# Performance work log

Hardware: AMD Instinct MI355X
Metric: run time of the kernel (lower is better)

The kernel has to match this reference:

```python
import jax, jax.numpy as jnp
import numpy as np

NUM_USERS = 100_000
NUM_ITEMS = 50_000
D = 64           # input_dim
K = 3            # num_weights (basis diagonal weights)
C = 5            # num_classes
E = 2_000_000    # number of (user, item) edges


def setup_inputs() -> dict:
    key = jax.random.key(0)
    ks = jax.random.split(key, 8)
    he = np.sqrt(2.0 / D).astype(np.float32)  # he_normal scale for [*, D] weights
    return {
        "u_feat": jax.random.normal(ks[0], (NUM_USERS, D), dtype=jnp.float32),
        "v_feat": jax.random.normal(ks[1], (NUM_ITEMS, D), dtype=jnp.float32),
        "W": jax.random.normal(ks[2], (K, D), dtype=jnp.float32) * he,
        "scalars": jax.random.normal(ks[3], (K, C), dtype=jnp.float32) * np.sqrt(2.0 / K).astype(np.float32),
        "u_bias": jnp.zeros((NUM_USERS, C), dtype=jnp.float32) + 0.01 * jax.random.normal(ks[4], (NUM_USERS, C), dtype=jnp.float32),
        "v_bias": jnp.zeros((NUM_ITEMS, C), dtype=jnp.float32) + 0.01 * jax.random.normal(ks[5], (NUM_ITEMS, C), dtype=jnp.float32),
        "u_idx": jax.random.randint(ks[6], (E,), 0, NUM_USERS, dtype=jnp.int32),
        "v_idx": jax.random.randint(ks[7], (E,), 0, NUM_ITEMS, dtype=jnp.int32),
    }


def reference(u_feat, v_feat, W, scalars, u_bias, v_bias, u_idx, v_idx):
    # Gather per-edge user/item embedding rows: [E, D]
    u_g = u_feat[u_idx]
    v_g = v_feat[v_idx]
    # Diagonal bilinear form per basis k: sum_d u_d * W[k,d] * v_d
    # = (u * v) @ W^T  -> basis_outputs: [E, K]
    basis_outputs = (u_g * v_g) @ W.T
    # Combine bases into class logits: [E, C]
    outputs = basis_outputs @ scalars
    # user_item_bias=True: add gathered per-user / per-item class biases
    outputs = outputs + u_bias[u_idx] + v_bias[v_idx]
    # activation=None -> linear
    return outputs
```

## Files before the change

### kernel.cpp

```cpp
#include <hip/hip_runtime.h>


template <int CTRL>
__device__ __forceinline__ float dpp_add(float x) {
    int t = __builtin_amdgcn_update_dpp(0, __float_as_int(x), CTRL, 0xF, 0xF, true);
    return x + __int_as_float(t);
}
template <int CTRL>
__device__ __forceinline__ float dpp_max(float x) {
    int t = __builtin_amdgcn_update_dpp(0, __float_as_int(x), CTRL, 0xF, 0xF, true);
    return fmaxf(x, __int_as_float(t));
}

__device__ __forceinline__ void reduce16_3(float& a, float& b, float& c) {
    a = dpp_add<0xB1>(a);  b = dpp_add<0xB1>(b);  c = dpp_add<0xB1>(c);
    a = dpp_add<0x4E>(a);  b = dpp_add<0x4E>(b);  c = dpp_add<0x4E>(c);
    a = dpp_add<0x124>(a); b = dpp_add<0x124>(b); c = dpp_add<0x124>(c);
    a = dpp_add<0x128>(a); b = dpp_add<0x128>(b); c = dpp_add<0x128>(c);
}
__device__ __forceinline__ float reduce16_max(float x) {
    x = dpp_max<0xB1>(x); x = dpp_max<0x4E>(x);
    x = dpp_max<0x124>(x); x = dpp_max<0x128>(x);
    return x;
}

__global__ __launch_bounds__(256) void quantize_tables_i8(
    const float* __restrict__ u_feat, const float* __restrict__ v_feat,
    int* __restrict__ u_q, int* __restrict__ v_q,
    float* __restrict__ u_s, float* __restrict__ v_s,
    int nrow_u, int nrow_v)
{
    const int tid   = blockIdx.x * blockDim.x + threadIdx.x;
    const int sl    = threadIdx.x & 15;
    const int group = tid >> 4;
    const int ng    = (gridDim.x * blockDim.x) >> 4;
    const int ntot  = nrow_u + nrow_v;

    for (int r = group; r < ntot; r += ng) {
        const bool  isU = (r < nrow_u);
        const int   rr  = isU ? r : r - nrow_u;
        const float* src = (isU ? u_feat : v_feat) + (size_t)rr * 64 + sl * 4;
        const float4 x = *reinterpret_cast<const float4*>(src);

        float am = fmaxf(fmaxf(fabsf(x.x), fabsf(x.y)),
                         fmaxf(fabsf(x.z), fabsf(x.w)));
        am = reduce16_max(am);
        am = fmaxf(am, 1e-20f);
        const float inv   = 127.0f / am;
        const float scale = am / 127.0f;

        const int b0 = (int)rintf(x.x * inv);
        const int b1 = (int)rintf(x.y * inv);
        const int b2 = (int)rintf(x.z * inv);
        const int b3 = (int)rintf(x.w * inv);
        const int packed = (b0 & 255) | ((b1 & 255) << 8) |
                           ((b2 & 255) << 16) | ((b3 & 255) << 24);

        (isU ? u_q : v_q)[(size_t)rr * 16 + sl] = packed;
        if (sl == 0) (isU ? u_s : v_s)[rr] = scale;
    }
}

__device__ __forceinline__ void unpack4(int t, float& f0, float& f1, float& f2, float& f3) {
    f0 = (float)((t << 24) >> 24);
    f1 = (float)((t << 16) >> 24);
    f2 = (float)((t <<  8) >> 24);
    f3 = (float)( t        >> 24);
}

__global__ __launch_bounds__(256) void bilinear_edges_i8(
    const int* __restrict__ u_q, const int* __restrict__ v_q,
    const float* __restrict__ u_s, const float* __restrict__ v_s,
    const float* __restrict__ W, const float* __restrict__ scalars,
    const float* __restrict__ u_bias, const float* __restrict__ v_bias,
    const int* __restrict__ u_idx, const int* __restrict__ v_idx,
    float* __restrict__ out, int E)
{
    const int tid    = blockIdx.x * blockDim.x + threadIdx.x;
    const int sl     = threadIdx.x & 15;
    const int group  = tid >> 4;
    const int ngroup = (gridDim.x * blockDim.x) >> 4;
    const int step   = ngroup * 2;

    const int d0 = sl * 4;
    float w0[4], w1[4], w2[4];
    #pragma unroll
    for (int j = 0; j < 4; ++j) {
        w0[j] = W[0 * 64 + d0 + j];
        w1[j] = W[1 * 64 + d0 + j];
        w2[j] = W[2 * 64 + d0 + j];
    }
    float s0 = 0.f, s1 = 0.f, s2 = 0.f;
    if (sl < 5) { s0 = scalars[0 * 5 + sl]; s1 = scalars[1 * 5 + sl]; s2 = scalars[2 * 5 + sl]; }

    int e0 = group * 2;
    if (e0 >= E) return;

    int uu0 = u_idx[e0];
    int vv0 = v_idx[e0];
    int uu1 = (e0 + 1 < E) ? u_idx[e0 + 1] : uu0;
    int vv1 = (e0 + 1 < E) ? v_idx[e0 + 1] : vv0;

    for (; e0 < E; e0 += step) {
        const int  e1   = e0 + 1;
        const bool has1 = (e1 < E);
        const int cu0 = uu0, cv0 = vv0, cu1 = uu1, cv1 = vv1;

        const int qu0 = u_q[(size_t)cu0 * 16 + sl];
        const int qv0 = v_q[(size_t)cv0 * 16 + sl];
        const int qu1 = u_q[(size_t)cu1 * 16 + sl];
        const int qv1 = v_q[(size_t)cv1 * 16 + sl];

        const int en = e0 + step;
        if (en < E) {
            uu0 = u_idx[en];
            vv0 = v_idx[en];
            const int en1 = en + 1;
            uu1 = (en1 < E) ? u_idx[en1] : uu0;
            vv1 = (en1 < E) ? v_idx[en1] : vv0;
        }

        float ub0 = 0.f, vb0 = 0.f, ub1 = 0.f, vb1 = 0.f;
        float ss0 = 0.f, ss1 = 0.f;
        if (sl < 5) {
            ss0 = u_s[cu0] * v_s[cv0];
            ss1 = u_s[cu1] * v_s[cv1];
            ub0 = u_bias[(size_t)cu0 * 5 + sl];
            vb0 = v_bias[(size_t)cv0 * 5 + sl];
            ub1 = u_bias[(size_t)cu1 * 5 + sl];
            vb1 = v_bias[(size_t)cv1 * 5 + sl];
        }

        float ua0, ua1, ua2, ua3, va0, va1, va2, va3;
        float ub0f, ub1f, ub2f, ub3f, vb0f, vb1f, vb2f, vb3f;
        unpack4(qu0, ua0, ua1, ua2, ua3);
        unpack4(qv0, va0, va1, va2, va3);
        unpack4(qu1, ub0f, ub1f, ub2f, ub3f);
        unpack4(qv1, vb0f, vb1f, vb2f, vb3f);

        const float a0 = ua0 * va0, a1 = ua1 * va1, a2 = ua2 * va2, a3 = ua3 * va3;
        const float b0 = ub0f * vb0f, b1 = ub1f * vb1f, b2 = ub2f * vb2f, b3 = ub3f * vb3f;

        float qa0 = a0*w0[0] + a1*w0[1] + a2*w0[2] + a3*w0[3];
        float qa1 = a0*w1[0] + a1*w1[1] + a2*w1[2] + a3*w1[3];
        float qa2 = a0*w2[0] + a1*w2[1] + a2*w2[2] + a3*w2[3];
        float qb0 = b0*w0[0] + b1*w0[1] + b2*w0[2] + b3*w0[3];
        float qb1 = b0*w1[0] + b1*w1[1] + b2*w1[2] + b3*w1[3];
        float qb2 = b0*w2[0] + b1*w2[1] + b2*w2[2] + b3*w2[3];

        reduce16_3(qa0, qa1, qa2);
        reduce16_3(qb0, qb1, qb2);

        if (sl < 5) {
            out[(size_t)e0 * 5 + sl] = (qa0 * s0 + qa1 * s1 + qa2 * s2) * ss0 + ub0 + vb0;
            if (has1)
                out[(size_t)e1 * 5 + sl] = (qb0 * s0 + qb1 * s1 + qb2 * s2) * ss1 + ub1 + vb1;
        }
    }
}

__global__ __launch_bounds__(256) void bilinear_edges_f32(
    const float* __restrict__ u_feat, const float* __restrict__ v_feat,
    const float* __restrict__ W, const float* __restrict__ scalars,
    const float* __restrict__ u_bias, const float* __restrict__ v_bias,
    const int* __restrict__ u_idx, const int* __restrict__ v_idx,
    float* __restrict__ out, int E)
{
    const int tid    = blockIdx.x * blockDim.x + threadIdx.x;
    const int sl     = threadIdx.x & 15;
    const int group  = tid >> 4;
    const int ngroup = (gridDim.x * blockDim.x) >> 4;

    const int d0 = sl * 4;
    float w0[4], w1[4], w2[4];
    #pragma unroll
    for (int j = 0; j < 4; ++j) {
        w0[j] = W[0 * 64 + d0 + j];
        w1[j] = W[1 * 64 + d0 + j];
        w2[j] = W[2 * 64 + d0 + j];
    }
    float s0 = 0.f, s1 = 0.f, s2 = 0.f;
    if (sl < 5) { s0 = scalars[0 * 5 + sl]; s1 = scalars[1 * 5 + sl]; s2 = scalars[2 * 5 + sl]; }

    for (int e = group; e < E; e += ngroup) {
        const int uu = u_idx[e];
        const int vv = v_idx[e];
        const float4 u4 = *reinterpret_cast<const float4*>(u_feat + (size_t)uu * 64 + d0);
        const float4 v4 = *reinterpret_cast<const float4*>(v_feat + (size_t)vv * 64 + d0);
        float ub = 0.f, vb = 0.f;
        if (sl < 5) { ub = u_bias[(size_t)uu * 5 + sl]; vb = v_bias[(size_t)vv * 5 + sl]; }

        const float p0 = u4.x * v4.x, p1 = u4.y * v4.y,
                    p2 = u4.z * v4.z, p3 = u4.w * v4.w;
        float q0 = p0*w0[0] + p1*w0[1] + p2*w0[2] + p3*w0[3];
        float q1 = p0*w1[0] + p1*w1[1] + p2*w1[2] + p3*w1[3];
        float q2 = p0*w2[0] + p1*w2[1] + p2*w2[2] + p3*w2[3];
        reduce16_3(q0, q1, q2);
        if (sl < 5)
            out[(size_t)e * 5 + sl] = q0 * s0 + q1 * s1 + q2 * s2 + ub + vb;
    }
}

extern "C" void kernel_launch(void* const* d_in, const int* in_sizes, int n_in,
                              void* d_out, int out_size, void* d_ws, size_t ws_size,
                              hipStream_t stream) {
    const float* u_feat  = (const float*)d_in[0];
    const float* v_feat  = (const float*)d_in[1];
    const float* W       = (const float*)d_in[2];
    const float* scalars = (const float*)d_in[3];
    const float* u_bias  = (const float*)d_in[4];
    const float* v_bias  = (const float*)d_in[5];
    const int*   u_idx   = (const int*)d_in[6];
    const int*   v_idx   = (const int*)d_in[7];
    float*       out     = (float*)d_out;

    const int nu = in_sizes[0];
    const int nv = in_sizes[1];
    const int E  = in_sizes[6];
    const int nrow_u = nu / 64;
    const int nrow_v = nv / 64;

    const size_t q_ints  = (size_t)(nrow_u + nrow_v) * 16;
    const size_t ws_need = q_ints * sizeof(int)
                         + (size_t)(nrow_u + nrow_v) * sizeof(float);

    if (ws_size >= ws_need) {
        int*   u_q = (int*)d_ws;
        int*   v_q = u_q + (size_t)nrow_u * 16;
        float* u_s = (float*)(v_q + (size_t)nrow_v * 16);
        float* v_s = u_s + nrow_u;

        quantize_tables_i8<<<2048, 256, 0, stream>>>(
            u_feat, v_feat, u_q, v_q, u_s, v_s, nrow_u, nrow_v);
        bilinear_edges_i8<<<2048, 256, 0, stream>>>(
            u_q, v_q, u_s, v_s, W, scalars, u_bias, v_bias, u_idx, v_idx, out, E);
    } else {
        bilinear_edges_f32<<<2048, 256, 0, stream>>>(
            u_feat, v_feat, W, scalars, u_bias, v_bias, u_idx, v_idx, out, E);
    }
}
```

Measured before the change: 209.1 us.

## Bin edges by user index and process bins per XCD for cache locality

Adds a three-kernel counting sort (per-block histogram, single-block prefix, scatter) that groups edges into 512 bins by user index. The compute kernel is replaced by a binned version that maps bins to blocks by XCD, so each die's L2 sees a narrower slice of the quantized user table. The aim is to cut scattered gather traffic to the user rows. In exchange it adds extra passes over the index arrays and writes permuted edge buffers, and the output stores become scattered by original edge id.

```diff
diff --git a/kernel.cpp b/kernel.cpp
--- a/kernel.cpp
+++ b/kernel.cpp
@@ -1,5 +1,8 @@
 #include <hip/hip_runtime.h>
 
+
+#define NBINS   512
+#define NBLK_HS 256
 
 template <int CTRL>
 __device__ __forceinline__ float dpp_add(float x) {
@@ -11,7 +14,6 @@
     int t = __builtin_amdgcn_update_dpp(0, __float_as_int(x), CTRL, 0xF, 0xF, true);
     return fmaxf(x, __int_as_float(t));
 }
-
 __device__ __forceinline__ void reduce16_3(float& a, float& b, float& c) {
     a = dpp_add<0xB1>(a);  b = dpp_add<0xB1>(b);  c = dpp_add<0xB1>(c);
     a = dpp_add<0x4E>(a);  b = dpp_add<0x4E>(b);  c = dpp_add<0x4E>(c);
@@ -61,85 +63,147 @@
     }
 }
 
-__device__ __forceinline__ void unpack4(int t, float& f0, float& f1, float& f2, float& f3) {
-    f0 = (float)((t << 24) >> 24);
-    f1 = (float)((t << 16) >> 24);
-    f2 = (float)((t <<  8) >> 24);
-    f3 = (float)( t        >> 24);
-}
-
-__global__ __launch_bounds__(256) void bilinear_edges_i8(
+__global__ __launch_bounds__(256) void edge_hist(
+    const int* __restrict__ u_idx, int E, float binScale,
+    int* __restrict__ hist )
+{
+    __shared__ int h[NBINS];
+    for (int i = threadIdx.x; i < NBINS; i += 256) h[i] = 0;
+    __syncthreads();
+    const int chunk = (E + NBLK_HS - 1) / NBLK_HS;
+    const int s = blockIdx.x * chunk;
+    const int e = min(E, s + chunk);
+    for (int i = s + threadIdx.x; i < e; i += 256) {
+        int b = min(NBINS - 1, (int)((float)u_idx[i] * binScale));
+        atomicAdd(&h[b], 1);
+    }
+    __syncthreads();
+    for (int i = threadIdx.x; i < NBINS; i += 256)
+        hist[blockIdx.x * NBINS + i] = h[i];
+}
+
+__global__ __launch_bounds__(256) void edge_prefix(
+    const int* __restrict__ hist, int* __restrict__ off,
+    int* __restrict__ binStart, int E)
+{
+    __shared__ int tot[NBINS];
+    __shared__ int start[NBINS + 1];
+    for (int b = threadIdx.x; b < NBINS; b += 256) {
+        int t = 0;
+        #pragma unroll 8
+        for (int k = 0; k < NBLK_HS; ++k) t += hist[k * NBINS + b];
+        tot[b] = t;
+    }
+    __syncthreads();
+    if (threadIdx.x == 0) {
+        int acc = 0;
+        for (int b = 0; b < NBINS; ++b) { start[b] = acc; acc += tot[b]; }
+        start[NBINS] = acc;
+    }
+    __syncthreads();
+    for (int b = threadIdx.x; b < NBINS; b += 256) {
+        int acc = start[b];
+        for (int k = 0; k < NBLK_HS; ++k) {
+            off[k * NBINS + b] = acc;
+            acc += hist[k * NBINS + b];
+        }
+    }
+    for (int b = threadIdx.x; b <= NBINS; b += 256) binStart[b] = start[b];
+}
+
+__global__ __launch_bounds__(256) void edge_scatter(
+    const int* __restrict__ u_idx, const int* __restrict__ v_idx,
+    int E, float binScale, const int* __restrict__ off,
+    int2* __restrict__ buv, int* __restrict__ bedge)
+{
+    __shared__ int cur[NBINS];
+    for (int i = threadIdx.x; i < NBINS; i += 256)
+        cur[i] = off[blockIdx.x * NBINS + i];
+    __syncthreads();
+    const int chunk = (E + NBLK_HS - 1) / NBLK_HS;
+    const int s = blockIdx.x * chunk;
+    const int e = min(E, s + chunk);
+    for (int i = s + threadIdx.x; i < e; i += 256) {
+        const int u = u_idx[i];
+        const int v = v_idx[i];
+        const int b = min(NBINS - 1, (int)((float)u * binScale));
+        const int p = atomicAdd(&cur[b], 1);
+        buv[p]   = make_int2(u, v);
+        bedge[p] = i;
+    }
+}
+
+__global__ __launch_bounds__(256) void bilinear_binned_i8(
     const int* __restrict__ u_q, const int* __restrict__ v_q,
     const float* __restrict__ u_s, const float* __restrict__ v_s,
     const float* __restrict__ W, const float* __restrict__ scalars,
     const float* __restrict__ u_bias, const float* __restrict__ v_bias,
-    const int* __restrict__ u_idx, const int* __restrict__ v_idx,
-    float* __restrict__ out, int E)
-{
-    const int tid    = blockIdx.x * blockDim.x + threadIdx.x;
-    const int sl     = threadIdx.x & 15;
-    const int group  = tid >> 4;
-    const int ngroup = (gridDim.x * blockDim.x) >> 4;
-    const int step   = ngroup * 2;
+    const int2* __restrict__ buv, const int* __restrict__ bedge,
+    const int* __restrict__ binStart, float* __restrict__ out)
+{
+    const int sl = threadIdx.x & 15;
+    const int g  = threadIdx.x >> 4;
+
+    const int B   = blockIdx.x;
+    const int xcd = B & 7;
+    const int j   = B >> 3;
+    const int bin = xcd + 8 * (j >> 2);
+    const int sub = j & 3;
+    const int bs  = binStart[bin];
+    const int be  = binStart[bin + 1];
+    const int cnt = be - bs;
+    const int q   = (cnt + 3) >> 2;
+    const int cs  = bs + sub * q;
+    const int ce  = min(be, cs + q);
+    if (cs >= ce) return;
 
     const int d0 = sl * 4;
     float w0[4], w1[4], w2[4];
     #pragma unroll
-    for (int j = 0; j < 4; ++j) {
-        w0[j] = W[0 * 64 + d0 + j];
-        w1[j] = W[1 * 64 + d0 + j];
-        w2[j] = W[2 * 64 + d0 + j];
+    for (int t = 0; t < 4; ++t) {
+        w0[t] = W[0 * 64 + d0 + t];
+        w1[t] = W[1 * 64 + d0 + t];
+        w2[t] = W[2 * 64 + d0 + t];
     }
     float s0 = 0.f, s1 = 0.f, s2 = 0.f;
     if (sl < 5) { s0 = scalars[0 * 5 + sl]; s1 = scalars[1 * 5 + sl]; s2 = scalars[2 * 5 + sl]; }
 
-    int e0 = group * 2;
-    if (e0 >= E) return;
-
-    int uu0 = u_idx[e0];
-    int vv0 = v_idx[e0];
-    int uu1 = (e0 + 1 < E) ? u_idx[e0 + 1] : uu0;
-    int vv1 = (e0 + 1 < E) ? v_idx[e0 + 1] : vv0;
-
-    for (; e0 < E; e0 += step) {
-        const int  e1   = e0 + 1;
-        const bool has1 = (e1 < E);
-        const int cu0 = uu0, cv0 = vv0, cu1 = uu1, cv1 = vv1;
-
-        const int qu0 = u_q[(size_t)cu0 * 16 + sl];
-        const int qv0 = v_q[(size_t)cv0 * 16 + sl];
-        const int qu1 = u_q[(size_t)cu1 * 16 + sl];
-        const int qv1 = v_q[(size_t)cv1 * 16 + sl];
-
-        const int en = e0 + step;
-        if (en < E) {
-            uu0 = u_idx[en];
-            vv0 = v_idx[en];
-            const int en1 = en + 1;
-            uu1 = (en1 < E) ? u_idx[en1] : uu0;
-            vv1 = (en1 < E) ? v_idx[en1] : vv0;
-        }
+    for (int p0 = cs + g * 2; p0 < ce; p0 += 32) {
+        const int  p1   = p0 + 1;
+        const bool has1 = (p1 < ce);
+
+        const int2 uv0 = buv[p0];
+        const int2 uv1 = has1 ? buv[p1] : uv0;
+        const int  e0  = bedge[p0];
+        const int  e1  = has1 ? bedge[p1] : e0;
+
+        const int qu0 = u_q[(size_t)uv0.x * 16 + sl];
+        const int qv0 = v_q[(size_t)uv0.y * 16 + sl];
+        const int qu1 = u_q[(size_t)uv1.x * 16 + sl];
+        const int qv1 = v_q[(size_t)uv1.y * 16 + sl];
 
         float ub0 = 0.f, vb0 = 0.f, ub1 = 0.f, vb1 = 0.f;
         float ss0 = 0.f, ss1 = 0.f;
         if (sl < 5) {
-            ss0 = u_s[cu0] * v_s[cv0];
-            ss1 = u_s[cu1] * v_s[cv1];
-            ub0 = u_bias[(size_t)cu0 * 5 + sl];
-            vb0 = v_bias[(size_t)cv0 * 5 + sl];
-            ub1 = u_bias[(size_t)cu1 * 5 + sl];
-            vb1 = v_bias[(size_t)cv1 * 5 + sl];
+            ss0 = u_s[uv0.x] * v_s[uv0.y];
+            ss1 = u_s[uv1.x] * v_s[uv1.y];
+            ub0 = u_bias[(size_t)uv0.x * 5 + sl];
+            vb0 = v_bias[(size_t)uv0.y * 5 + sl];
+            ub1 = u_bias[(size_t)uv1.x * 5 + sl];
+            vb1 = v_bias[(size_t)uv1.y * 5 + sl];
         }
 
-        float ua0, ua1, ua2, ua3, va0, va1, va2, va3;
-        float ub0f, ub1f, ub2f, ub3f, vb0f, vb1f, vb2f, vb3f;
-        unpack4(qu0, ua0, ua1, ua2, ua3);
-        unpack4(qv0, va0, va1, va2, va3);
-        unpack4(qu1, ub0f, ub1f, ub2f, ub3f);
-        unpack4(qv1, vb0f, vb1f, vb2f, vb3f);
+        float ua0 = (float)((qu0 << 24) >> 24), ua1 = (float)((qu0 << 16) >> 24),
+              ua2 = (float)((qu0 <<  8) >> 24), ua3 = (float)( qu0        >> 24);
+        float va0 = (float)((qv0 << 24) >> 24), va1 = (float)((qv0 << 16) >> 24),
+              va2 = (float)((qv0 <<  8) >> 24), va3 = (float)( qv0        >> 24);
+        float xb0 = (float)((qu1 << 24) >> 24), xb1 = (float)((qu1 << 16) >> 24),
+              xb2 = (float)((qu1 <<  8) >> 24), xb3 = (float)( qu1        >> 24);
+        float yb0 = (float)((qv1 << 24) >> 24), yb1 = (float)((qv1 << 16) >> 24),
+              yb2 = (float)((qv1 <<  8) >> 24), yb3 = (float)( qv1        >> 24);
 
         const float a0 = ua0 * va0, a1 = ua1 * va1, a2 = ua2 * va2, a3 = ua3 * va3;
-        const float b0 = ub0f * vb0f, b1 = ub1f * vb1f, b2 = ub2f * vb2f, b3 = ub3f * vb3f;
+        const float b0 = xb0 * yb0, b1 = xb1 * yb1, b2 = xb2 * yb2, b3 = xb3 * yb3;
 
         float qa0 = a0*w0[0] + a1*w0[1] + a2*w0[2] + a3*w0[3];
         float qa1 = a0*w1[0] + a1*w1[1] + a2*w1[2] + a3*w1[3];
@@ -174,10 +238,10 @@
     const int d0 = sl * 4;
     float w0[4], w1[4], w2[4];
     #pragma unroll
-    for (int j = 0; j < 4; ++j) {
-        w0[j] = W[0 * 64 + d0 + j];
-        w1[j] = W[1 * 64 + d0 + j];
-        w2[j] = W[2 * 64 + d0 + j];
+    for (int t = 0; t < 4; ++t) {
+        w0[t] = W[0 * 64 + d0 + t];
+        w1[t] = W[1 * 64 + d0 + t];
+        w2[t] = W[2 * 64 + d0 + t];
     }
     float s0 = 0.f, s1 = 0.f, s2 = 0.f;
     if (sl < 5) { s0 = scalars[0 * 5 + sl]; s1 = scalars[1 * 5 + sl]; s2 = scalars[2 * 5 + sl]; }
@@ -220,20 +284,36 @@
     const int nrow_u = nu / 64;
     const int nrow_v = nv / 64;
 
-    const size_t q_ints  = (size_t)(nrow_u + nrow_v) * 16;
-    const size_t ws_need = q_ints * sizeof(int)
-                         + (size_t)(nrow_u + nrow_v) * sizeof(float);
-
-    if (ws_size >= ws_need) {
-        int*   u_q = (int*)d_ws;
-        int*   v_q = u_q + (size_t)nrow_u * 16;
-        float* u_s = (float*)(v_q + (size_t)nrow_v * 16);
-        float* v_s = u_s + nrow_u;
+    const size_t need =
+        (size_t)E * 8 +
+        (size_t)(nrow_u + nrow_v) * 16 * 4 +
+        (size_t)(nrow_u + nrow_v) * 4 +
+        (size_t)E * 4 +
+        (size_t)2 * NBLK_HS * NBINS * 4 +
+        (size_t)(NBINS + 1) * 4;
+
+    if (ws_size >= need) {
+        int2* buv      = (int2*)d_ws;
+        int*  u_q      = (int*)(buv + E);
+        int*  v_q      = u_q + (size_t)nrow_u * 16;
+        float* u_s     = (float*)(v_q + (size_t)nrow_v * 16);
+        float* v_s     = u_s + nrow_u;
+        int*  bedge    = (int*)(v_s + nrow_v);
+        int*  hist     = bedge + E;
+        int*  off      = hist + (size_t)NBLK_HS * NBINS;
+        int*  binStart = off + (size_t)NBLK_HS * NBINS;
+
+        const float binScale = (float)NBINS / (float)nrow_u;
 
         quantize_tables_i8<<<2048, 256, 0, stream>>>(
             u_feat, v_feat, u_q, v_q, u_s, v_s, nrow_u, nrow_v);
-        bilinear_edges_i8<<<2048, 256, 0, stream>>>(
-            u_q, v_q, u_s, v_s, W, scalars, u_bias, v_bias, u_idx, v_idx, out, E);
+        edge_hist<<<NBLK_HS, 256, 0, stream>>>(u_idx, E, binScale, hist);
+        edge_prefix<<<1, 256, 0, stream>>>(hist, off, binStart, E);
+        edge_scatter<<<NBLK_HS, 256, 0, stream>>>(
+            u_idx, v_idx, E, binScale, off, buv, bedge);
+        bilinear_binned_i8<<<2048, 256, 0, stream>>>(
+            u_q, v_q, u_s, v_s, W, scalars, u_bias, v_bias,
+            buv, bedge, binStart, out);
     } else {
         bilinear_edges_f32<<<2048, 256, 0, stream>>>(
             u_feat, v_feat, W, scalars, u_bias, v_bias, u_idx, v_idx, out, E);
```

Measured after the change: 302.9 us. +44.9%, slower.

## Pack int8 features, scale and bias into one 128-byte row per entity

Applied to the files above, without the earlier changes.

Replaces the separate int8 feature table, per-row scale array and bias gathers with a single 128-byte packed row per user/item. Lanes 0-7 hold 8 int8 features each, lanes 8-12 hold a (bias, scale) pair, and lanes 13-15 are zero padding. Each edge now gathers one cache-line-sized row per side instead of several scattered loads, which should cut random-access transactions. In exchange, the packing kernel is slightly larger, half the lanes do no arithmetic, and lanes 8-15 each handle 8 bytes of metadata.

```diff
diff --git a/kernel.cpp b/kernel.cpp
--- a/kernel.cpp
+++ b/kernel.cpp
@@ -1,5 +1,7 @@
 #include <hip/hip_runtime.h>
 
+
+#define ROWB 128
 
 template <int CTRL>
 __device__ __forceinline__ float dpp_add(float x) {
@@ -11,7 +13,6 @@
     int t = __builtin_amdgcn_update_dpp(0, __float_as_int(x), CTRL, 0xF, 0xF, true);
     return fmaxf(x, __int_as_float(t));
 }
-
 __device__ __forceinline__ void reduce16_3(float& a, float& b, float& c) {
     a = dpp_add<0xB1>(a);  b = dpp_add<0xB1>(b);  c = dpp_add<0xB1>(c);
     a = dpp_add<0x4E>(a);  b = dpp_add<0x4E>(b);  c = dpp_add<0x4E>(c);
@@ -24,55 +25,65 @@
     return x;
 }
 
-__global__ __launch_bounds__(256) void quantize_tables_i8(
+__device__ __forceinline__ void unpack4i8(int t, float* f) {
+    f[0] = (float)((t << 24) >> 24);
+    f[1] = (float)((t << 16) >> 24);
+    f[2] = (float)((t <<  8) >> 24);
+    f[3] = (float)( t        >> 24);
+}
+
+__global__ __launch_bounds__(256) void pack_rows(
     const float* __restrict__ u_feat, const float* __restrict__ v_feat,
-    int* __restrict__ u_q, int* __restrict__ v_q,
-    float* __restrict__ u_s, float* __restrict__ v_s,
-    int nrow_u, int nrow_v)
+    const float* __restrict__ u_bias, const float* __restrict__ v_bias,
+    char* __restrict__ u_p, char* __restrict__ v_p, int nru, int nrv)
 {
     const int tid   = blockIdx.x * blockDim.x + threadIdx.x;
     const int sl    = threadIdx.x & 15;
     const int group = tid >> 4;
     const int ng    = (gridDim.x * blockDim.x) >> 4;
-    const int ntot  = nrow_u + nrow_v;
+    const int ntot  = nru + nrv;
 
     for (int r = group; r < ntot; r += ng) {
-        const bool  isU = (r < nrow_u);
-        const int   rr  = isU ? r : r - nrow_u;
-        const float* src = (isU ? u_feat : v_feat) + (size_t)rr * 64 + sl * 4;
-        const float4 x = *reinterpret_cast<const float4*>(src);
-
-        float am = fmaxf(fmaxf(fabsf(x.x), fabsf(x.y)),
-                         fmaxf(fabsf(x.z), fabsf(x.w)));
+        const bool isU = (r < nru);
+        const int  rr  = isU ? r : r - nru;
+        const float* src = (isU ? u_feat : v_feat) + (size_t)rr * 64;
+
+        float x[8];
+        float am = 0.f;
+        if (sl < 8) {
+            const float4 a = *reinterpret_cast<const float4*>(src + sl * 8);
+            const float4 b = *reinterpret_cast<const float4*>(src + sl * 8 + 4);
+            x[0]=a.x; x[1]=a.y; x[2]=a.z; x[3]=a.w;
+            x[4]=b.x; x[5]=b.y; x[6]=b.z; x[7]=b.w;
+            #pragma unroll
+            for (int j = 0; j < 8; ++j) am = fmaxf(am, fabsf(x[j]));
+        }
         am = reduce16_max(am);
         am = fmaxf(am, 1e-20f);
         const float inv   = 127.0f / am;
         const float scale = am / 127.0f;
 
-        const int b0 = (int)rintf(x.x * inv);
-        const int b1 = (int)rintf(x.y * inv);
-        const int b2 = (int)rintf(x.z * inv);
-        const int b3 = (int)rintf(x.w * inv);
-        const int packed = (b0 & 255) | ((b1 & 255) << 8) |
-                           ((b2 & 255) << 16) | ((b3 & 255) << 24);
-
-        (isU ? u_q : v_q)[(size_t)rr * 16 + sl] = packed;
-        if (sl == 0) (isU ? u_s : v_s)[rr] = scale;
-    }
-}
-
-__device__ __forceinline__ void unpack4(int t, float& f0, float& f1, float& f2, float& f3) {
-    f0 = (float)((t << 24) >> 24);
-    f1 = (float)((t << 16) >> 24);
-    f2 = (float)((t <<  8) >> 24);
-    f3 = (float)( t        >> 24);
-}
-
-__global__ __launch_bounds__(256) void bilinear_edges_i8(
-    const int* __restrict__ u_q, const int* __restrict__ v_q,
-    const float* __restrict__ u_s, const float* __restrict__ v_s,
+        char* row = (isU ? u_p : v_p) + (size_t)rr * ROWB;
+        if (sl < 8) {
+            int b[8];
+            #pragma unroll
+            for (int j = 0; j < 8; ++j) b[j] = (int)rintf(x[j] * inv) & 255;
+            const int lo = b[0] | (b[1] << 8) | (b[2] << 16) | (b[3] << 24);
+            const int hi = b[4] | (b[5] << 8) | (b[6] << 16) | (b[7] << 24);
+            reinterpret_cast<int2*>(row)[sl] = make_int2(lo, hi);
+        } else if (sl < 13) {
+            const int   cc = sl - 8;
+            const float bb = (isU ? u_bias : v_bias)[(size_t)rr * 5 + cc];
+            reinterpret_cast<float2*>(row)[sl] = make_float2(bb, scale);
+        } else {
+            reinterpret_cast<float2*>(row)[sl] = make_float2(0.f, 0.f);
+        }
+    }
+}
+
+__global__ __launch_bounds__(256) void bilinear_packed(
+    const char* __restrict__ u_p, const char* __restrict__ v_p,
     const float* __restrict__ W, const float* __restrict__ scalars,
-    const float* __restrict__ u_bias, const float* __restrict__ v_bias,
     const int* __restrict__ u_idx, const int* __restrict__ v_idx,
     float* __restrict__ out, int E)
 {
@@ -82,16 +93,24 @@
     const int ngroup = (gridDim.x * blockDim.x) >> 4;
     const int step   = ngroup * 2;
 
-    const int d0 = sl * 4;
-    float w0[4], w1[4], w2[4];
+    const bool lead   = (sl < 8);
+    const bool writer = (sl >= 8) && (sl < 13);
+    const int  c      = sl - 8;
+
+    float w0[8], w1[8], w2[8];
     #pragma unroll
-    for (int j = 0; j < 4; ++j) {
-        w0[j] = W[0 * 64 + d0 + j];
-        w1[j] = W[1 * 64 + d0 + j];
-        w2[j] = W[2 * 64 + d0 + j];
+    for (int j = 0; j < 8; ++j) { w0[j] = 0.f; w1[j] = 0.f; w2[j] = 0.f; }
+    if (lead) {
+        const int d0 = sl * 8;
+        #pragma unroll
+        for (int j = 0; j < 8; ++j) {
+            w0[j] = W[d0 + j];
+            w1[j] = W[64 + d0 + j];
+            w2[j] = W[128 + d0 + j];
+        }
     }
     float s0 = 0.f, s1 = 0.f, s2 = 0.f;
-    if (sl < 5) { s0 = scalars[0 * 5 + sl]; s1 = scalars[1 * 5 + sl]; s2 = scalars[2 * 5 + sl]; }
+    if (writer) { s0 = scalars[c]; s1 = scalars[5 + c]; s2 = scalars[10 + c]; }
 
     int e0 = group * 2;
     if (e0 >= E) return;
@@ -106,55 +125,54 @@
         const bool has1 = (e1 < E);
         const int cu0 = uu0, cv0 = vv0, cu1 = uu1, cv1 = vv1;
 
-        const int qu0 = u_q[(size_t)cu0 * 16 + sl];
-        const int qv0 = v_q[(size_t)cv0 * 16 + sl];
-        const int qu1 = u_q[(size_t)cu1 * 16 + sl];
-        const int qv1 = v_q[(size_t)cv1 * 16 + sl];
-
-        const int en = e0 + step;
-        if (en < E) {
-            uu0 = u_idx[en];
-            vv0 = v_idx[en];
-            const int en1 = en + 1;
-            uu1 = (en1 < E) ? u_idx[en1] : uu0;
-            vv1 = (en1 < E) ? v_idx[en1] : vv0;
-        }
-
-        float ub0 = 0.f, vb0 = 0.f, ub1 = 0.f, vb1 = 0.f;
-        float ss0 = 0.f, ss1 = 0.f;
-        if (sl < 5) {
-            ss0 = u_s[cu0] * v_s[cv0];
-            ss1 = u_s[cu1] * v_s[cv1];
-            ub0 = u_bias[(size_t)cu0 * 5 + sl];
-            vb0 = v_bias[(size_t)cv0 * 5 + sl];
-            ub1 = u_bias[(size_t)cu1 * 5 + sl];
-            vb1 = v_bias[(size_t)cv1 * 5 + sl];
-        }
-
-        float ua0, ua1, ua2, ua3, va0, va1, va2, va3;
-        float ub0f, ub1f, ub2f, ub3f, vb0f, vb1f, vb2f, vb3f;
-        unpack4(qu0, ua0, ua1, ua2, ua3);
-        unpack4(qv0, va0, va1, va2, va3);
-        unpack4(qu1, ub0f, ub1f, ub2f, ub3f);
-        unpack4(qv1, vb0f, vb1f, vb2f, vb3f);
-
-        const float a0 = ua0 * va0, a1 = ua1 * va1, a2 = ua2 * va2, a3 = ua3 * va3;
-        const float b0 = ub0f * vb0f, b1 = ub1f * vb1f, b2 = ub2f * vb2f, b3 = ub3f * vb3f;
-
-        float qa0 = a0*w0[0] + a1*w0[1] + a2*w0[2] + a3*w0[3];
-        float qa1 = a0*w1[0] + a1*w1[1] + a2*w1[2] + a3*w1[3];
-        float qa2 = a0*w2[0] + a1*w2[1] + a2*w2[2] + a3*w2[3];
-        float qb0 = b0*w0[0] + b1*w0[1] + b2*w0[2] + b3*w0[3];
-        float qb1 = b0*w1[0] + b1*w1[1] + b2*w1[2] + b3*w1[3];
-        float qb2 = b0*w2[0] + b1*w2[1] + b2*w2[2] + b3*w2[3];
+        const int2 Ua = *reinterpret_cast<const int2*>(u_p + (size_t)cu0 * ROWB + sl * 8);
+        const int2 Va = *reinterpret_cast<const int2*>(v_p + (size_t)cv0 * ROWB + sl * 8);
+        const int2 Ub = *reinterpret_cast<const int2*>(u_p + (size_t)cu1 * ROWB + sl * 8);
+        const int2 Vb = *reinterpret_cast<const int2*>(v_p + (size_t)cv1 * ROWB + sl * 8);
+
+        const int nb = e0 + step;
+        if (nb < E) {
+            uu0 = u_idx[nb];
+            vv0 = v_idx[nb];
+            const int nb1 = nb + 1;
+            uu1 = (nb1 < E) ? u_idx[nb1] : uu0;
+            vv1 = (nb1 < E) ? v_idx[nb1] : vv0;
+        }
+
+        float qa0 = 0.f, qa1 = 0.f, qa2 = 0.f;
+        float qb0 = 0.f, qb1 = 0.f, qb2 = 0.f;
+        if (lead) {
+            float fu[8], fv[8];
+            unpack4i8(Ua.x, fu); unpack4i8(Ua.y, fu + 4);
+            unpack4i8(Va.x, fv); unpack4i8(Va.y, fv + 4);
+            #pragma unroll
+            for (int j = 0; j < 8; ++j) {
+                const float p = fu[j] * fv[j];
+                qa0 += p * w0[j]; qa1 += p * w1[j]; qa2 += p * w2[j];
+            }
+            unpack4i8(Ub.x, fu); unpack4i8(Ub.y, fu + 4);
+            unpack4i8(Vb.x, fv); unpack4i8(Vb.y, fv + 4);
+            #pragma unroll
+            for (int j = 0; j < 8; ++j) {
+                const float p = fu[j] * fv[j];
+                qb0 += p * w0[j]; qb1 += p * w1[j]; qb2 += p * w2[j];
+            }
+        }
 
         reduce16_3(qa0, qa1, qa2);
         reduce16_3(qb0, qb1, qb2);
 
-        if (sl < 5) {
-            out[(size_t)e0 * 5 + sl] = (qa0 * s0 + qa1 * s1 + qa2 * s2) * ss0 + ub0 + vb0;
-            if (has1)
-                out[(size_t)e1 * 5 + sl] = (qb0 * s0 + qb1 * s1 + qb2 * s2) * ss1 + ub1 + vb1;
+        if (writer) {
+            const float bu0 = __int_as_float(Ua.x), su0 = __int_as_float(Ua.y);
+            const float bv0 = __int_as_float(Va.x), sv0 = __int_as_float(Va.y);
+            out[(size_t)e0 * 5 + c] =
+                (qa0 * s0 + qa1 * s1 + qa2 * s2) * (su0 * sv0) + bu0 + bv0;
+            if (has1) {
+                const float bu1 = __int_as_float(Ub.x), su1 = __int_as_float(Ub.y);
+                const float bv1 = __int_as_float(Vb.x), sv1 = __int_as_float(Vb.y);
+                out[(size_t)e1 * 5 + c] =
+                    (qb0 * s0 + qb1 * s1 + qb2 * s2) * (su1 * sv1) + bu1 + bv1;
+            }
         }
     }
 }
@@ -174,21 +192,21 @@
     const int d0 = sl * 4;
     float w0[4], w1[4], w2[4];
     #pragma unroll
-    for (int j = 0; j < 4; ++j) {
-        w0[j] = W[0 * 64 + d0 + j];
-        w1[j] = W[1 * 64 + d0 + j];
-        w2[j] = W[2 * 64 + d0 + j];
+    for (int t = 0; t < 4; ++t) {
+        w0[t] = W[0 * 64 + d0 + t];
+        w1[t] = W[1 * 64 + d0 + t];
+        w2[t] = W[2 * 64 + d0 + t];
     }
     float s0 = 0.f, s1 = 0.f, s2 = 0.f;
-    if (sl < 5) { s0 = scalars[0 * 5 + sl]; s1 = scalars[1 * 5 + sl]; s2 = scalars[2 * 5 + sl]; }
+    if (sl < 5) { s0 = scalars[sl]; s1 = scalars[5 + sl]; s2 = scalars[10 + sl]; }
 
     for (int e = group; e < E; e += ngroup) {
         const int uu = u_idx[e];
         const int vv = v_idx[e];
         const float4 u4 = *reinterpret_cast<const float4*>(u_feat + (size_t)uu * 64 + d0);
         const float4 v4 = *reinterpret_cast<const float4*>(v_feat + (size_t)vv * 64 + d0);
-        float ub = 0.f, vb = 0.f;
-        if (sl < 5) { ub = u_bias[(size_t)uu * 5 + sl]; vb = v_bias[(size_t)vv * 5 + sl]; }
+        float ubx = 0.f, vbx = 0.f;
+        if (sl < 5) { ubx = u_bias[(size_t)uu * 5 + sl]; vbx = v_bias[(size_t)vv * 5 + sl]; }
 
         const float p0 = u4.x * v4.x, p1 = u4.y * v4.y,
                     p2 = u4.z * v4.z, p3 = u4.w * v4.w;
@@ -197,7 +215,7 @@
         float q2 = p0*w2[0] + p1*w2[1] + p2*w2[2] + p3*w2[3];
         reduce16_3(q0, q1, q2);
         if (sl < 5)
-            out[(size_t)e * 5 + sl] = q0 * s0 + q1 * s1 + q2 * s2 + ub + vb;
+            out[(size_t)e * 5 + sl] = q0 * s0 + q1 * s1 + q2 * s2 + ubx + vbx;
     }
 }
 
@@ -217,23 +235,18 @@
     const int nu = in_sizes[0];
     const int nv = in_sizes[1];
     const int E  = in_sizes[6];
-    const int nrow_u = nu / 64;
-    const int nrow_v = nv / 64;
-
-    const size_t q_ints  = (size_t)(nrow_u + nrow_v) * 16;
-    const size_t ws_need = q_ints * sizeof(int)
-                         + (size_t)(nrow_u + nrow_v) * sizeof(float);
+    const int nru = nu / 64;
+    const int nrv = nv / 64;
+
+    const size_t ws_need = (size_t)(nru + nrv) * ROWB;
 
     if (ws_size >= ws_need) {
-        int*   u_q = (int*)d_ws;
-        int*   v_q = u_q + (size_t)nrow_u * 16;
-        float* u_s = (float*)(v_q + (size_t)nrow_v * 16);
-        float* v_s = u_s + nrow_u;
-
-        quantize_tables_i8<<<2048, 256, 0, stream>>>(
-            u_feat, v_feat, u_q, v_q, u_s, v_s, nrow_u, nrow_v);
-        bilinear_edges_i8<<<2048, 256, 0, stream>>>(
-            u_q, v_q, u_s, v_s, W, scalars, u_bias, v_bias, u_idx, v_idx, out, E);
+        char* u_p = (char*)d_ws;
+        char* v_p = u_p + (size_t)nru * ROWB;
+        pack_rows<<<2048, 256, 0, stream>>>(
+            u_feat, v_feat, u_bias, v_bias, u_p, v_p, nru, nrv);
+        bilinear_packed<<<2048, 256, 0, stream>>>(
+            u_p, v_p, W, scalars, u_idx, v_idx, out, E);
     } else {
         bilinear_edges_f32<<<2048, 256, 0, stream>>>(
             u_feat, v_feat, W, scalars, u_bias, v_bias, u_idx, v_idx, out, E);
```

Result: slower. 221.9 us (+6.1%).
